# Performance work log

Hardware: AMD Instinct MI355X
Metric: run time of the kernel (lower is better)

## Reference

```python
import jax, jax.numpy as jnp
import numpy as np

B, S, H, NH = 2, 2048, 1024, 4
DH = H // NH
EPS = 1e-6


def setup_inputs() -> dict:
    key = jax.random.key(0)
    ks = jax.random.split(key, 6)
    q = jax.random.normal(ks[0], (B, S, H), dtype=jnp.float32)
    k = jax.random.normal(ks[1], (B, S, H), dtype=jnp.float32)
    v = jax.random.normal(ks[2], (B, S, H), dtype=jnp.float32)
    # gate projections: Linear(3*H -> NH). Kernels are zero-init in the module;
    # use small random kernels so the projection path is exercised.
    igate_kernel = jax.random.normal(ks[3], (3 * H, NH), dtype=jnp.float32) * 0.02
    fgate_kernel = jax.random.normal(ks[4], (3 * H, NH), dtype=jnp.float32) * 0.02
    igate_bias = jax.random.normal(ks[5], (NH,), dtype=jnp.float32) * 0.1
    fgate_bias = jnp.linspace(3.0, 6.0, NH, dtype=jnp.float32)  # bias_linspace_initializer
    outnorm_scale = jnp.ones((H,), dtype=jnp.float32)  # MultiHeadLayerNorm scale, no bias
    return {"q": q, "k": k, "v": v,
            "igate_kernel": igate_kernel, "igate_bias": igate_bias,
            "fgate_kernel": fgate_kernel, "fgate_bias": fgate_bias,
            "outnorm_scale": outnorm_scale}


def _parallel_stabilized(qh, kh, vh, ig, fg):
    # qh,kh,vh: (B,NH,S,DH); ig,fg: (B,NH,S,1) gate preactivations
    log_fg = jax.nn.log_sigmoid(fg)                      # (B,NH,S,1)
    cs = jnp.cumsum(log_fg, axis=2)                      # cumulative log forget gates
    ltr = jnp.tril(jnp.ones((qh.shape[2], qh.shape[2]), dtype=bool))
    # log decay matrix: sum_{t=j+1}^{i} log f_t = cs[i] - cs[j], masked causal
    log_fg_mat = jnp.where(ltr, cs - jnp.swapaxes(cs, 2, 3), -jnp.inf)  # (B,NH,S,S)
    log_D = log_fg_mat + jnp.swapaxes(ig, 2, 3)          # add input gate per column
    max_log_D = jnp.max(log_D, axis=-1, keepdims=True)   # row-wise stabilizer
    D = jnp.exp(log_D - max_log_D)                       # (B,NH,S,S)
    qk = jnp.einsum("bhsd,bhtd->bhst", qh, kh) / jnp.sqrt(jnp.float32(DH))
    C = qk * D
    normalizer = jnp.maximum(jnp.abs(jnp.sum(C, axis=-1, keepdims=True)),
                             jnp.exp(-max_log_D))
    return jnp.einsum("bhst,bhtd->bhsd", C / (normalizer + EPS), vh)


def reference(q, k, v, igate_kernel, igate_bias, fgate_kernel, fgate_bias, outnorm_scale):
    Bq, Sq, Hq = q.shape
    x = jnp.concatenate([q, k, v], axis=-1)              # (B,S,3H)
    ig = (x @ igate_kernel + igate_bias)                 # (B,S,NH)
    fg = (x @ fgate_kernel + fgate_bias)
    ig = jnp.transpose(ig, (0, 2, 1))[..., None]         # (B,NH,S,1)
    fg = jnp.transpose(fg, (0, 2, 1))[..., None]
    qh = jnp.transpose(q.reshape(Bq, Sq, NH, DH), (0, 2, 1, 3))
    kh = jnp.transpose(k.reshape(Bq, Sq, NH, DH), (0, 2, 1, 3))
    vh = jnp.transpose(v.reshape(Bq, Sq, NH, DH), (0, 2, 1, 3))
    h = _parallel_stabilized(qh, kh, vh, ig, fg)         # (B,NH,S,DH)
    # MultiHeadLayerNorm: per-head layernorm over DH, scale only
    mean = jnp.mean(h, axis=-1, keepdims=True)
    var = jnp.mean((h - mean) ** 2, axis=-1, keepdims=True)
    h_norm = (h - mean) * jax.lax.rsqrt(var + 1e-5)
    h_norm = h_norm * outnorm_scale.reshape(1, NH, 1, DH)
    out = jnp.transpose(h_norm, (0, 2, 1, 3)).reshape(Bq, Sq, Hq)
    return out
```

## Files before the change

kernel.cpp:

```cpp
#include <hip/hip_runtime.h>
#include <hip/hip_bf16.h>


#define S_LEN 2048
#define DHD   256
#define NHEAD 4
#define BATCH 2
#define HID   1024
#define BH_CNT (BATCH*NHEAD)

typedef __attribute__((ext_vector_type(8))) short bf16x8;
typedef __attribute__((ext_vector_type(4))) short short4v;
typedef __attribute__((ext_vector_type(4))) float f32x4;

static __device__ __forceinline__ short f2b(float f) {
  __hip_bfloat16 h = __float2bfloat16(f);
  return *reinterpret_cast<short*>(&h);
}

static __device__ __forceinline__ bf16x8 pack8(f32x4 a, f32x4 b) {
  bf16x8 o;
  o[0]=f2b(a[0]); o[1]=f2b(a[1]); o[2]=f2b(a[2]); o[3]=f2b(a[3]);
  o[4]=f2b(b[0]); o[5]=f2b(b[1]); o[6]=f2b(b[2]); o[7]=f2b(b[3]);
  return o;
}

static __device__ __forceinline__ void gload16(const void* src, void* ldsdst) {
  __builtin_amdgcn_global_load_lds(
      (const __attribute__((address_space(1))) void*)src,
      (__attribute__((address_space(3))) void*)ldsdst, 16, 0, 0);
}

__global__ __launch_bounds__(256) void prep_kernel(
    const float* __restrict__ q, const float* __restrict__ k, const float* __restrict__ v,
    const float* __restrict__ wi, const float* __restrict__ wf,
    short* __restrict__ Kg, short* __restrict__ Vg,
    float* __restrict__ igA, float* __restrict__ fgA) {
  __shared__ short vt2[32][264];
  const int bx = blockIdx.x, t = threadIdx.x;
  if (bx < 768) {
    const int w = t >> 6, lane = t & 63;
    const int gw = bx*4 + w;
    const int seg = gw % 3;
    const int rg = gw / 3;
    const float* xp = (seg == 0) ? q : (seg == 1) ? k : v;
    const float* wip = wi + (long)seg*HID*NHEAD;
    const float* wfp = wf + (long)seg*HID*NHEAD;
    f32x4 ai[4], af[4];
#pragma unroll
    for (int r = 0; r < 4; r++) { ai[r] = f32x4{0,0,0,0}; af[r] = f32x4{0,0,0,0}; }
    for (int cb = 0; cb < HID; cb += 64) {
      const int c = cb + lane;
      const f32x4 wiv = *(const f32x4*)(wip + (long)c*NHEAD);
      const f32x4 wfv = *(const f32x4*)(wfp + (long)c*NHEAD);
#pragma unroll
      for (int r = 0; r < 4; r++) {
        const float x = xp[(long)(rg*4 + r)*HID + c];
        ai[r] += x * wiv;
        af[r] += x * wfv;
      }
    }
#pragma unroll
    for (int mk = 32; mk >= 1; mk >>= 1)
#pragma unroll
      for (int r = 0; r < 4; r++)
#pragma unroll
        for (int e = 0; e < 4; e++) {
          ai[r][e] += __shfl_xor(ai[r][e], mk);
          af[r][e] += __shfl_xor(af[r][e], mk);
        }
    if (lane == 0) {
#pragma unroll
      for (int r = 0; r < 4; r++) {
        const long row = rg*4 + r;
#pragma unroll
        for (int e = 0; e < 4; e++) {
          unsafeAtomicAdd(&igA[row*NHEAD + e], ai[r][e]);
          unsafeAtomicAdd(&fgA[row*NHEAD + e], af[r][e]);
        }
      }
    }
  } else if (bx < 2816) {
    const int kb = bx - 768;
    const int g_row = kb*2 + (t >> 7);
    const int col = (t & 127) * 8;
    const long off = (long)g_row*HID + col;
    const f32x4 xk0 = *(const f32x4*)(k + off);
    const f32x4 xk1 = *(const f32x4*)(k + off + 4);
    bf16x8 o = pack8(xk0, xk1);
    const int b = g_row >> 11, s = g_row & (S_LEN-1);
    const int hh = col >> 8, d = col & 255;
    const int bh = b*NHEAD + hh, jt = s >> 5, rr = s & 31;
    *(bf16x8*)(Kg + ((long)bh*64 + jt)*8192 + rr*256 + (d ^ ((rr & 7) << 3))) = o;
  } else {
    const int t2 = bx - 2816;
    const int jt = t2 & 63, bhv = t2 >> 6;
    const int b = bhv >> 2, hh = bhv & 3;
    const int j0 = jt * 32;
    const int r0 = t >> 3, c0 = (t & 7) * 32;
    const float* vsrc = v + ((long)(b*S_LEN + j0 + r0))*HID + hh*DHD + c0;
#pragma unroll
    for (int i = 0; i < 4; i++) {
      f32x4 a  = *(const f32x4*)(vsrc + i*8);
      f32x4 bb = *(const f32x4*)(vsrc + i*8 + 4);
      *(bf16x8*)&vt2[r0][c0 + i*8] = pack8(a, bb);
    }
    __syncthreads();
    const long base = ((long)bhv*64 + jt) * 8192;
    const int j = t & 31, dg = t >> 5;
#pragma unroll
    for (int dd = 0; dd < 32; dd++) {
      const int d = dg*32 + dd;
      Vg[base + (long)d*32 + (j ^ (((d >> 1) & 3) << 3))] = vt2[j][d];
    }
  }
}

__global__ void scan_kernel(const float* __restrict__ ig, const float* __restrict__ fg,
                            const float* __restrict__ bi, const float* __restrict__ bf_,
                            float* __restrict__ a_out, float* __restrict__ m_out,
                            float* __restrict__ nf_out) {
  int bh = blockIdx.x, b = bh >> 2, h = bh & 3;
  int t = threadIdx.x;
  __shared__ float tot[256];
  long gbase = (long)b * S_LEN;
  const float biv = bi[h], bfv = bf_[h];
  float ls[8];
  float run = 0.f;
  for (int e = 0; e < 8; e++) {
    int s = t*8 + e;
    float x = fg[(gbase + s)*NHEAD + h] + bfv;
    float l = fminf(x, 0.f) - log1pf(expf(-fabsf(x)));
    run += l; ls[e] = run;
  }
  tot[t] = run;
  __syncthreads();
  for (int off = 1; off < 256; off <<= 1) {
    float x = tot[t];
    if (t >= off) x += tot[t - off];
    __syncthreads();
    tot[t] = x;
    __syncthreads();
  }
  float offc = (t == 0) ? 0.f : tot[t-1];
  __syncthreads();
  float av[8], am[8], csv[8];
  float runm = -1e30f;
  for (int e = 0; e < 8; e++) {
    int s = t*8 + e;
    float cs = ls[e] + offc;
    csv[e] = cs;
    float a = (ig[(gbase + s)*NHEAD + h] + biv) - cs;
    av[e] = a;
    runm = fmaxf(runm, a);
    am[e] = runm;
  }
  tot[t] = runm;
  __syncthreads();
  for (int off = 1; off < 256; off <<= 1) {
    float x = tot[t];
    if (t >= off) x = fmaxf(x, tot[t - off]);
    __syncthreads();
    tot[t] = x;
    __syncthreads();
  }
  float offm = (t == 0) ? -1e30f : tot[t-1];
  long obase = (long)bh * S_LEN;
  for (int e = 0; e < 8; e++) {
    int s = t*8 + e;
    float mm = fmaxf(am[e], offm);
    a_out[obase + s]  = av[e];
    m_out[obase + s]  = mm;
    nf_out[obase + s] = expf(-(csv[e] + mm));
  }
}

__global__ __launch_bounds__(256, 1) void mlstm_main_kernel(
    const float* __restrict__ q, const short* __restrict__ Kg, const short* __restrict__ Vg,
    const float* __restrict__ a_arr, const float* __restrict__ m_arr,
    const float* __restrict__ nf_arr, const float* __restrict__ lns,
    float* __restrict__ outp) {
  __shared__ alignas(16) short Kst[2][2][8192];
  __shared__ alignas(16) short Vst[2][2][8192];
  __shared__ alignas(16) short plds[4][16*36];
  const int w = threadIdx.x >> 6, lane = threadIdx.x & 63;
  const int lr = lane & 15, g = lane >> 4;
  const int rg2 = w >> 1, kp = w & 1;
  const int bh = blockIdx.x & 7, it = blockIdx.x >> 3;
  const int b = bh >> 2, h = bh & 3;
  const int R0 = it*64 + rg2*32;
  const long arow = (long)bh * S_LEN;
  const int np = it + 1;
  const int ntw = it*2 + rg2 + 1;
  const f32x4 zz = {0.f,0.f,0.f,0.f};
  const int sw = (lr & 7) << 3;

  bf16x8 qfa[8], qfb[8];
  const float* qsrc = q + ((long)(b*S_LEN + R0 + lr))*HID + h*DHD + g*8;
#pragma unroll
  for (int c8 = 0; c8 < 8; c8++) {
    f32x4 u0 = *(const f32x4*)(qsrc + c8*32);
    f32x4 u1 = *(const f32x4*)(qsrc + c8*32 + 4);
    f32x4 w0 = *(const f32x4*)(qsrc + 16*HID + c8*32);
    f32x4 w1 = *(const f32x4*)(qsrc + 16*HID + c8*32 + 4);
    qfa[c8] = pack8(u0, u1);
    qfb[c8] = pack8(w0, w1);
  }
  float ma[4], mb[4];
#pragma unroll
  for (int r = 0; r < 4; r++) {
    ma[r] = m_arr[arow + R0 + g*4 + r];
    mb[r] = m_arr[arow + R0 + 16 + g*4 + r];
  }

  f32x4 oa[16], ob[16];
#pragma unroll
  for (int t = 0; t < 16; t++) { oa[t] = zz; ob[t] = zz; }
  float rs_a[4] = {0,0,0,0}, rs_b[4] = {0,0,0,0};
  short* myp = plds[w];

  auto STAGE = [&](int pb, int p) {
    const int jts = 2*p + (w & 1);
    short* dst = (w < 2) ? &Kst[pb][w & 1][0] : &Vst[pb][w & 1][0];
    const short* src = ((w < 2) ? Kg : Vg) + ((long)bh*64 + jts)*8192 + lane*8;
#pragma unroll
    for (int u = 0; u < 16; u++)
      gload16(src + u*512, dst + u*512);
  };

  float aC0, aC1, aN0 = 0.f, aN1 = 0.f;
  STAGE(0, 0);
  { const int j0 = kp*32;
    aC0 = a_arr[arow + j0 + lr]; aC1 = a_arr[arow + j0 + 16 + lr]; }

  for (int p = 0; p < np; ++p) {
    const int pb = p & 1;
    if (p + 1 < np) {
      STAGE(pb ^ 1, p + 1);
      { const int j0 = (2*(p+1) + kp)*32;
        aN0 = a_arr[arow + j0 + lr]; aN1 = a_arr[arow + j0 + 16 + lr]; }
      asm volatile("s_waitcnt vmcnt(16)" ::: "memory");
    } else {
      asm volatile("s_waitcnt vmcnt(0)" ::: "memory");
    }
    __builtin_amdgcn_s_barrier();

    const int jtc = 2*p + kp;
    if (jtc < ntw) {
      const int j0 = jtc*32;
      const short* Kt = &Kst[pb][kp][0];
      const short* Vt = &Vst[pb][kp][0];
      f32x4 s0a = zz, s1a = zz, s0b = zz, s1b = zz;
      __builtin_amdgcn_s_setprio(1);
#pragma unroll
      for (int c8 = 0; c8 < 8; c8++) {
        const int ko = lr*256 + ((c8*32 + g*8) ^ sw);
        bf16x8 k0 = *(const bf16x8*)&Kt[ko];
        bf16x8 k1 = *(const bf16x8*)&Kt[ko + 4096];
        s0a = __builtin_amdgcn_mfma_f32_16x16x32_bf16(qfa[c8], k0, s0a, 0, 0, 0);
        s0b = __builtin_amdgcn_mfma_f32_16x16x32_bf16(qfb[c8], k0, s0b, 0, 0, 0);
        s1a = __builtin_amdgcn_mfma_f32_16x16x32_bf16(qfa[c8], k1, s1a, 0, 0, 0);
        s1b = __builtin_amdgcn_mfma_f32_16x16x32_bf16(qfb[c8], k1, s1b, 0, 0, 0);
      }
      __builtin_amdgcn_s_setprio(0);
      bf16x8 pa_a, pa_b;
      {
        const bool needmask = (j0 + 31 > R0);
#pragma unroll
        for (int r = 0; r < 4; r++) {
          const int i = R0 + g*4 + r;
          float p0 = s0a[r] * 0.0625f * __expf(aC0 - ma[r]);
          float p1 = s1a[r] * 0.0625f * __expf(aC1 - ma[r]);
          if (needmask) {
            if (j0 + lr > i)      p0 = 0.f;
            if (j0 + 16 + lr > i) p1 = 0.f;
          }
          rs_a[r] += p0 + p1;
          myp[(g*4 + r)*36 + lr]      = f2b(p0);
          myp[(g*4 + r)*36 + 16 + lr] = f2b(p1);
        }
        const short* rp = myp + lr*36 + g*8;
        short4v plo = *(const short4v*)rp;
        short4v phi = *(const short4v*)(rp + 4);
        pa_a = bf16x8{plo[0],plo[1],plo[2],plo[3],phi[0],phi[1],phi[2],phi[3]};
      }
      {
        const bool needmask = (j0 + 31 > R0 + 16);
#pragma unroll
        for (int r = 0; r < 4; r++) {
          const int i = R0 + 16 + g*4 + r;
          float p0 = s0b[r] * 0.0625f * __expf(aC0 - mb[r]);
          float p1 = s1b[r] * 0.0625f * __expf(aC1 - mb[r]);
          if (needmask) {
            if (j0 + lr > i)      p0 = 0.f;
            if (j0 + 16 + lr > i) p1 = 0.f;
          }
          rs_b[r] += p0 + p1;
          myp[(g*4 + r)*36 + lr]      = f2b(p0);
          myp[(g*4 + r)*36 + 16 + lr] = f2b(p1);
        }
        const short* rp = myp + lr*36 + g*8;
        short4v plo = *(const short4v*)rp;
        short4v phi = *(const short4v*)(rp + 4);
        pa_b = bf16x8{plo[0],plo[1],plo[2],plo[3],phi[0],phi[1],phi[2],phi[3]};
      }
      __builtin_amdgcn_s_setprio(1);
#pragma unroll
      for (int t = 0; t < 16; t++) {
        const int d = t*16 + lr;
        const int vo = d*32 + ((g*8) ^ (((d >> 1) & 3) << 3));
        bf16x8 vf = *(const bf16x8*)&Vt[vo];
        oa[t] = __builtin_amdgcn_mfma_f32_16x16x32_bf16(pa_a, vf, oa[t], 0, 0, 0);
        ob[t] = __builtin_amdgcn_mfma_f32_16x16x32_bf16(pa_b, vf, ob[t], 0, 0, 0);
      }
      __builtin_amdgcn_s_setprio(0);
    }
    __builtin_amdgcn_s_barrier();
    if (p + 1 < np) { aC0 = aN0; aC1 = aN1; }
  }

#pragma unroll
  for (int r = 0; r < 4; r++)
    for (int mk = 1; mk < 16; mk <<= 1) {
      rs_a[r] += __shfl_xor(rs_a[r], mk);
      rs_b[r] += __shfl_xor(rs_b[r], mk);
    }

  float* Ols = (float*)&Kst[0][0][0];
  float* rsl = (float*)&Vst[0][0][0];
  __syncthreads();
  if (kp == 1) {
#pragma unroll
    for (int r = 0; r < 4; r++) {
      const int rla = rg2*32 + g*4 + r, rlb = rla + 16;
#pragma unroll
      for (int t = 0; t < 16; t++) {
        Ols[(long)rla*256 + t*16 + lr] = oa[t][r];
        Ols[(long)rlb*256 + t*16 + lr] = ob[t][r];
      }
      if (lr == 0) { rsl[rla] = rs_a[r]; rsl[rlb] = rs_b[r]; }
    }
  }
  __syncthreads();
  if (kp == 0) {
    float sc[16];
#pragma unroll
    for (int t = 0; t < 16; t++) sc[t] = lns[h*DHD + t*16 + lr];
    for (int grp = 0; grp < 2; grp++) {
      f32x4* acc = grp ? ob : oa;
      float* rsv = grp ? rs_b : rs_a;
#pragma unroll
      for (int r = 0; r < 4; r++) {
        const int rl = rg2*32 + grp*16 + g*4 + r;
        const int i = R0 + grp*16 + g*4 + r;
        const float rst = rsv[r] + rsl[rl];
        const float nfv = nf_arr[arow + i];
        const float inv = 1.f / (fmaxf(fabsf(rst), nfv) + 1e-6f);
        float sum = 0.f, sq = 0.f;
        float xv[16];
#pragma unroll
        for (int t = 0; t < 16; t++) {
          float x = (acc[t][r] + Ols[(long)rl*256 + t*16 + lr]) * inv;
          xv[t] = x; sum += x; sq += x*x;
        }
        for (int mk = 1; mk < 16; mk <<= 1) {
          sum += __shfl_xor(sum, mk);
          sq  += __shfl_xor(sq,  mk);
        }
        const float mean = sum * (1.f/256.f);
        const float var  = sq * (1.f/256.f) - mean*mean;
        const float rstd = rsqrtf(var + 1e-5f);
        float* orow = outp + ((long)(b*S_LEN + i))*HID + h*DHD + lr;
#pragma unroll
        for (int t = 0; t < 16; t++)
          orow[t*16] = (xv[t] - mean) * rstd * sc[t];
      }
    }
  }
}

extern "C" void kernel_launch(void* const* d_in, const int* in_sizes, int n_in,
                              void* d_out, int out_size, void* d_ws, size_t ws_size,
                              hipStream_t stream) {
  const float* q   = (const float*)d_in[0];
  const float* k   = (const float*)d_in[1];
  const float* v   = (const float*)d_in[2];
  const float* wi  = (const float*)d_in[3];
  const float* bi  = (const float*)d_in[4];
  const float* wf  = (const float*)d_in[5];
  const float* bf_ = (const float*)d_in[6];
  const float* lns = (const float*)d_in[7];
  float* outp = (float*)d_out;

  char* ws = (char*)d_ws;
  const long nelem = (long)BH_CNT * S_LEN * DHD;
  short* Kg  = (short*)ws;
  short* Vg  = Kg + nelem;
  float* igA = (float*)(ws + 2*nelem*sizeof(short));
  float* fgA = igA + (long)BATCH*S_LEN*NHEAD;
  float* aA  = fgA + (long)BATCH*S_LEN*NHEAD;
  float* mA  = aA + (long)BH_CNT*S_LEN;
  float* nfA = mA + (long)BH_CNT*S_LEN;

  hipMemsetAsync(igA, 0, 2 * (size_t)BATCH*S_LEN*NHEAD * sizeof(float), stream);

  prep_kernel<<<3328, 256, 0, stream>>>(q, k, v, wi, wf, Kg, Vg, igA, fgA);
  scan_kernel<<<BH_CNT, 256, 0, stream>>>(igA, fgA, bi, bf_, aA, mA, nfA);
  mlstm_main_kernel<<<BH_CNT*32, 256, 0, stream>>>(q, Kg, Vg, aA, mA, nfA, lns, outp);
}
```

Baseline: 114.6 us.

## Split key-parity work across blocks with atomic accumulation and separate finalize kernel

The main attention kernel now launches twice as many blocks. Each handles one key-tile parity for a 64-row query tile, and each wave owns 16 rows instead of 32, which halves the register and LDS footprint and allows two blocks per CU. Partial outputs and row sums are combined with float atomics into the zeroed output and a row-sum buffer. A new finalize kernel then applies the normalizer and the per-head layernorm. This should improve occupancy and load balance (blocks are ordered heaviest first), at the cost of extra memsets, atomic traffic, another launch and a second pass over the output.

Result: faster. 110.8 us (-3.3%).

```diff
diff --git a/kernel.cpp b/kernel.cpp
--- a/kernel.cpp
+++ b/kernel.cpp
@@ -175,143 +175,115 @@
   }
 }
 
-__global__ __launch_bounds__(256, 1) void mlstm_main_kernel(
+__global__ __launch_bounds__(256, 2) void mlstm_partial_kernel(
     const float* __restrict__ q, const short* __restrict__ Kg, const short* __restrict__ Vg,
     const float* __restrict__ a_arr, const float* __restrict__ m_arr,
-    const float* __restrict__ nf_arr, const float* __restrict__ lns,
-    float* __restrict__ outp) {
-  __shared__ alignas(16) short Kst[2][2][8192];
-  __shared__ alignas(16) short Vst[2][2][8192];
+    float* __restrict__ outp, float* __restrict__ rsacc) {
+  __shared__ alignas(16) short Kst[2][8192];
+  __shared__ alignas(16) short Vst[2][8192];
   __shared__ alignas(16) short plds[4][16*36];
   const int w = threadIdx.x >> 6, lane = threadIdx.x & 63;
   const int lr = lane & 15, g = lane >> 4;
-  const int rg2 = w >> 1, kp = w & 1;
-  const int bh = blockIdx.x & 7, it = blockIdx.x >> 3;
+  int pi, it, bh;
+  if (blockIdx.x < 256) { pi = 0; bh = blockIdx.x & 7; it = 31 - (int)(blockIdx.x >> 3); }
+  else { const int j = blockIdx.x - 256; pi = 1; bh = j & 7; it = j >> 3; }
   const int b = bh >> 2, h = bh & 3;
-  const int R0 = it*64 + rg2*32;
+  const int R0 = it*64 + w*16;
   const long arow = (long)bh * S_LEN;
   const int np = it + 1;
-  const int ntw = it*2 + rg2 + 1;
+  const int dmax = 2*it + (w >> 1) - pi;
+  const int pmax = (dmax >= 0) ? (dmax >> 1) : -1;
   const f32x4 zz = {0.f,0.f,0.f,0.f};
   const int sw = (lr & 7) << 3;
 
-  bf16x8 qfa[8], qfb[8];
+  bf16x8 qf[8];
   const float* qsrc = q + ((long)(b*S_LEN + R0 + lr))*HID + h*DHD + g*8;
 #pragma unroll
   for (int c8 = 0; c8 < 8; c8++) {
     f32x4 u0 = *(const f32x4*)(qsrc + c8*32);
     f32x4 u1 = *(const f32x4*)(qsrc + c8*32 + 4);
-    f32x4 w0 = *(const f32x4*)(qsrc + 16*HID + c8*32);
-    f32x4 w1 = *(const f32x4*)(qsrc + 16*HID + c8*32 + 4);
-    qfa[c8] = pack8(u0, u1);
-    qfb[c8] = pack8(w0, w1);
-  }
-  float ma[4], mb[4];
-#pragma unroll
-  for (int r = 0; r < 4; r++) {
-    ma[r] = m_arr[arow + R0 + g*4 + r];
-    mb[r] = m_arr[arow + R0 + 16 + g*4 + r];
-  }
-
-  f32x4 oa[16], ob[16];
-#pragma unroll
-  for (int t = 0; t < 16; t++) { oa[t] = zz; ob[t] = zz; }
-  float rs_a[4] = {0,0,0,0}, rs_b[4] = {0,0,0,0};
+    qf[c8] = pack8(u0, u1);
+  }
+  float mrow[4];
+#pragma unroll
+  for (int r = 0; r < 4; r++) mrow[r] = m_arr[arow + R0 + g*4 + r];
+
+  f32x4 oacc[16];
+#pragma unroll
+  for (int t = 0; t < 16; t++) oacc[t] = zz;
+  float rs[4] = {0.f,0.f,0.f,0.f};
   short* myp = plds[w];
 
   auto STAGE = [&](int pb, int p) {
-    const int jts = 2*p + (w & 1);
-    short* dst = (w < 2) ? &Kst[pb][w & 1][0] : &Vst[pb][w & 1][0];
-    const short* src = ((w < 2) ? Kg : Vg) + ((long)bh*64 + jts)*8192 + lane*8;
-#pragma unroll
-    for (int u = 0; u < 16; u++)
-      gload16(src + u*512, dst + u*512);
+    const int jts = 2*p + pi;
+    const long toff = ((long)bh*64 + jts)*8192 + w*2048 + lane*8;
+    short* kdst = &Kst[pb][w*2048];
+    short* vdst = &Vst[pb][w*2048];
+    const short* ksrc = Kg + toff;
+    const short* vsrc = Vg + toff;
+#pragma unroll
+    for (int u = 0; u < 4; u++) gload16(ksrc + u*512, kdst + u*512);
+#pragma unroll
+    for (int u = 0; u < 4; u++) gload16(vsrc + u*512, vdst + u*512);
   };
 
   float aC0, aC1, aN0 = 0.f, aN1 = 0.f;
   STAGE(0, 0);
-  { const int j0 = kp*32;
+  { const int j0 = pi*32;
     aC0 = a_arr[arow + j0 + lr]; aC1 = a_arr[arow + j0 + 16 + lr]; }
 
   for (int p = 0; p < np; ++p) {
     const int pb = p & 1;
     if (p + 1 < np) {
       STAGE(pb ^ 1, p + 1);
-      { const int j0 = (2*(p+1) + kp)*32;
+      { const int j0 = (2*(p+1) + pi)*32;
         aN0 = a_arr[arow + j0 + lr]; aN1 = a_arr[arow + j0 + 16 + lr]; }
-      asm volatile("s_waitcnt vmcnt(16)" ::: "memory");
+      asm volatile("s_waitcnt vmcnt(8)" ::: "memory");
     } else {
       asm volatile("s_waitcnt vmcnt(0)" ::: "memory");
     }
     __builtin_amdgcn_s_barrier();
 
-    const int jtc = 2*p + kp;
-    if (jtc < ntw) {
-      const int j0 = jtc*32;
-      const short* Kt = &Kst[pb][kp][0];
-      const short* Vt = &Vst[pb][kp][0];
-      f32x4 s0a = zz, s1a = zz, s0b = zz, s1b = zz;
+    if (p <= pmax) {
+      const int j0 = (2*p + pi)*32;
+      const short* Kt = &Kst[pb][0];
+      const short* Vt = &Vst[pb][0];
+      f32x4 s0 = zz, s1 = zz;
       __builtin_amdgcn_s_setprio(1);
 #pragma unroll
       for (int c8 = 0; c8 < 8; c8++) {
         const int ko = lr*256 + ((c8*32 + g*8) ^ sw);
         bf16x8 k0 = *(const bf16x8*)&Kt[ko];
         bf16x8 k1 = *(const bf16x8*)&Kt[ko + 4096];
-        s0a = __builtin_amdgcn_mfma_f32_16x16x32_bf16(qfa[c8], k0, s0a, 0, 0, 0);
-        s0b = __builtin_amdgcn_mfma_f32_16x16x32_bf16(qfb[c8], k0, s0b, 0, 0, 0);
-        s1a = __builtin_amdgcn_mfma_f32_16x16x32_bf16(qfa[c8], k1, s1a, 0, 0, 0);
-        s1b = __builtin_amdgcn_mfma_f32_16x16x32_bf16(qfb[c8], k1, s1b, 0, 0, 0);
+        s0 = __builtin_amdgcn_mfma_f32_16x16x32_bf16(qf[c8], k0, s0, 0, 0, 0);
+        s1 = __builtin_amdgcn_mfma_f32_16x16x32_bf16(qf[c8], k1, s1, 0, 0, 0);
       }
       __builtin_amdgcn_s_setprio(0);
-      bf16x8 pa_a, pa_b;
-      {
-        const bool needmask = (j0 + 31 > R0);
-#pragma unroll
-        for (int r = 0; r < 4; r++) {
-          const int i = R0 + g*4 + r;
-          float p0 = s0a[r] * 0.0625f * __expf(aC0 - ma[r]);
-          float p1 = s1a[r] * 0.0625f * __expf(aC1 - ma[r]);
-          if (needmask) {
-            if (j0 + lr > i)      p0 = 0.f;
-            if (j0 + 16 + lr > i) p1 = 0.f;
-          }
-          rs_a[r] += p0 + p1;
-          myp[(g*4 + r)*36 + lr]      = f2b(p0);
-          myp[(g*4 + r)*36 + 16 + lr] = f2b(p1);
+      const bool needmask = (j0 + 31 > R0);
+#pragma unroll
+      for (int r = 0; r < 4; r++) {
+        const int i = R0 + g*4 + r;
+        float p0 = s0[r] * 0.0625f * __expf(aC0 - mrow[r]);
+        float p1 = s1[r] * 0.0625f * __expf(aC1 - mrow[r]);
+        if (needmask) {
+          if (j0 + lr > i)      p0 = 0.f;
+          if (j0 + 16 + lr > i) p1 = 0.f;
         }
-        const short* rp = myp + lr*36 + g*8;
-        short4v plo = *(const short4v*)rp;
-        short4v phi = *(const short4v*)(rp + 4);
-        pa_a = bf16x8{plo[0],plo[1],plo[2],plo[3],phi[0],phi[1],phi[2],phi[3]};
-      }
-      {
-        const bool needmask = (j0 + 31 > R0 + 16);
-#pragma unroll
-        for (int r = 0; r < 4; r++) {
-          const int i = R0 + 16 + g*4 + r;
-          float p0 = s0b[r] * 0.0625f * __expf(aC0 - mb[r]);
-          float p1 = s1b[r] * 0.0625f * __expf(aC1 - mb[r]);
-          if (needmask) {
-            if (j0 + lr > i)      p0 = 0.f;
-            if (j0 + 16 + lr > i) p1 = 0.f;
-          }
-          rs_b[r] += p0 + p1;
-          myp[(g*4 + r)*36 + lr]      = f2b(p0);
-          myp[(g*4 + r)*36 + 16 + lr] = f2b(p1);
-        }
-        const short* rp = myp + lr*36 + g*8;
-        short4v plo = *(const short4v*)rp;
-        short4v phi = *(const short4v*)(rp + 4);
-        pa_b = bf16x8{plo[0],plo[1],plo[2],plo[3],phi[0],phi[1],phi[2],phi[3]};
-      }
+        rs[r] += p0 + p1;
+        myp[(g*4 + r)*36 + lr]      = f2b(p0);
+        myp[(g*4 + r)*36 + 16 + lr] = f2b(p1);
+      }
+      const short* rp = myp + lr*36 + g*8;
+      short4v plo = *(const short4v*)rp;
+      short4v phi = *(const short4v*)(rp + 4);
+      bf16x8 pa = {plo[0],plo[1],plo[2],plo[3],phi[0],phi[1],phi[2],phi[3]};
       __builtin_amdgcn_s_setprio(1);
 #pragma unroll
       for (int t = 0; t < 16; t++) {
         const int d = t*16 + lr;
         const int vo = d*32 + ((g*8) ^ (((d >> 1) & 3) << 3));
         bf16x8 vf = *(const bf16x8*)&Vt[vo];
-        oa[t] = __builtin_amdgcn_mfma_f32_16x16x32_bf16(pa_a, vf, oa[t], 0, 0, 0);
-        ob[t] = __builtin_amdgcn_mfma_f32_16x16x32_bf16(pa_b, vf, ob[t], 0, 0, 0);
+        oacc[t] = __builtin_amdgcn_mfma_f32_16x16x32_bf16(pa, vf, oacc[t], 0, 0, 0);
       }
       __builtin_amdgcn_s_setprio(0);
     }
@@ -321,62 +293,48 @@
 
 #pragma unroll
   for (int r = 0; r < 4; r++)
-    for (int mk = 1; mk < 16; mk <<= 1) {
-      rs_a[r] += __shfl_xor(rs_a[r], mk);
-      rs_b[r] += __shfl_xor(rs_b[r], mk);
-    }
-
-  float* Ols = (float*)&Kst[0][0][0];
-  float* rsl = (float*)&Vst[0][0][0];
-  __syncthreads();
-  if (kp == 1) {
-#pragma unroll
-    for (int r = 0; r < 4; r++) {
-      const int rla = rg2*32 + g*4 + r, rlb = rla + 16;
-#pragma unroll
-      for (int t = 0; t < 16; t++) {
-        Ols[(long)rla*256 + t*16 + lr] = oa[t][r];
-        Ols[(long)rlb*256 + t*16 + lr] = ob[t][r];
-      }
-      if (lr == 0) { rsl[rla] = rs_a[r]; rsl[rlb] = rs_b[r]; }
-    }
-  }
-  __syncthreads();
-  if (kp == 0) {
-    float sc[16];
-#pragma unroll
-    for (int t = 0; t < 16; t++) sc[t] = lns[h*DHD + t*16 + lr];
-    for (int grp = 0; grp < 2; grp++) {
-      f32x4* acc = grp ? ob : oa;
-      float* rsv = grp ? rs_b : rs_a;
-#pragma unroll
-      for (int r = 0; r < 4; r++) {
-        const int rl = rg2*32 + grp*16 + g*4 + r;
-        const int i = R0 + grp*16 + g*4 + r;
-        const float rst = rsv[r] + rsl[rl];
-        const float nfv = nf_arr[arow + i];
-        const float inv = 1.f / (fmaxf(fabsf(rst), nfv) + 1e-6f);
-        float sum = 0.f, sq = 0.f;
-        float xv[16];
-#pragma unroll
-        for (int t = 0; t < 16; t++) {
-          float x = (acc[t][r] + Ols[(long)rl*256 + t*16 + lr]) * inv;
-          xv[t] = x; sum += x; sq += x*x;
-        }
-        for (int mk = 1; mk < 16; mk <<= 1) {
-          sum += __shfl_xor(sum, mk);
-          sq  += __shfl_xor(sq,  mk);
-        }
-        const float mean = sum * (1.f/256.f);
-        const float var  = sq * (1.f/256.f) - mean*mean;
-        const float rstd = rsqrtf(var + 1e-5f);
-        float* orow = outp + ((long)(b*S_LEN + i))*HID + h*DHD + lr;
-#pragma unroll
-        for (int t = 0; t < 16; t++)
-          orow[t*16] = (xv[t] - mean) * rstd * sc[t];
-      }
-    }
-  }
+    for (int mk = 1; mk < 16; mk <<= 1)
+      rs[r] += __shfl_xor(rs[r], mk);
+
+#pragma unroll
+  for (int r = 0; r < 4; r++) {
+    const int i = R0 + g*4 + r;
+    float* orow = outp + ((long)(b*S_LEN + i))*HID + h*DHD + lr;
+#pragma unroll
+    for (int t = 0; t < 16; t++)
+      unsafeAtomicAdd(orow + t*16, oacc[t][r]);
+    if (lr == 0)
+      unsafeAtomicAdd(&rsacc[arow + i], rs[r]);
+  }
+}
+
+__global__ __launch_bounds__(256) void finalize_kernel(
+    float* __restrict__ outp, const float* __restrict__ rsacc,
+    const float* __restrict__ nf_arr, const float* __restrict__ lns) {
+  const int bi = blockIdx.x;
+  const int h = threadIdx.x >> 6, lane = threadIdx.x & 63;
+  const int b = bi >> 11, i = bi & (S_LEN-1);
+  const int bh = b*NHEAD + h;
+  const long roff = (long)bi * HID + (long)h*DHD;
+  f32x4 xv = *(const f32x4*)(outp + roff + lane*4);
+  const float rsv = rsacc[(long)bh*S_LEN + i];
+  const float nfv = nf_arr[(long)bh*S_LEN + i];
+  const float inv = 1.f / (fmaxf(fabsf(rsv), nfv) + 1e-6f);
+  xv[0]*=inv; xv[1]*=inv; xv[2]*=inv; xv[3]*=inv;
+  float sum = xv[0]+xv[1]+xv[2]+xv[3];
+  float sq  = xv[0]*xv[0]+xv[1]*xv[1]+xv[2]*xv[2]+xv[3]*xv[3];
+  for (int mk = 1; mk < 64; mk <<= 1) {
+    sum += __shfl_xor(sum, mk);
+    sq  += __shfl_xor(sq,  mk);
+  }
+  const float mean = sum * (1.f/256.f);
+  const float var  = sq * (1.f/256.f) - mean*mean;
+  const float rstd = rsqrtf(var + 1e-5f);
+  f32x4 sc = *(const f32x4*)(lns + h*DHD + lane*4);
+  f32x4 o;
+  o[0]=(xv[0]-mean)*rstd*sc[0]; o[1]=(xv[1]-mean)*rstd*sc[1];
+  o[2]=(xv[2]-mean)*rstd*sc[2]; o[3]=(xv[3]-mean)*rstd*sc[3];
+  *(f32x4*)(outp + roff + lane*4) = o;
 }
 
 extern "C" void kernel_launch(void* const* d_in, const int* in_sizes, int n_in,
@@ -401,10 +359,14 @@
   float* aA  = fgA + (long)BATCH*S_LEN*NHEAD;
   float* mA  = aA + (long)BH_CNT*S_LEN;
   float* nfA = mA + (long)BH_CNT*S_LEN;
+  float* rsA = nfA + (long)BH_CNT*S_LEN;
 
   hipMemsetAsync(igA, 0, 2 * (size_t)BATCH*S_LEN*NHEAD * sizeof(float), stream);
+  hipMemsetAsync(outp, 0, (size_t)out_size * sizeof(float), stream);
+  hipMemsetAsync(rsA, 0, (size_t)BH_CNT * S_LEN * sizeof(float), stream);
 
   prep_kernel<<<3328, 256, 0, stream>>>(q, k, v, wi, wf, Kg, Vg, igA, fgA);
   scan_kernel<<<BH_CNT, 256, 0, stream>>>(igA, fgA, bi, bf_, aA, mA, nfA);
-  mlstm_main_kernel<<<BH_CNT*32, 256, 0, stream>>>(q, Kg, Vg, aA, mA, nfA, lns, outp);
-}
+  mlstm_partial_kernel<<<512, 256, 0, stream>>>(q, Kg, Vg, aA, mA, outp, rsA);
+  finalize_kernel<<<BATCH*S_LEN, 256, 0, stream>>>(outp, rsA, nfA, lns);
+}
```
